# Performance work log

Measured on AMD Instinct MI355X. Metric: run time of the kernel, lower is better.

## Reference

```python
import jax, jax.numpy as jnp
import numpy as np

SQRT_HALF = np.float32(np.sqrt(0.5))


def _weight_norm(v, g):
    # torch weight_norm dim=0: per-output-row normalization, w = g * v / ||v||_row
    return (g / jnp.linalg.norm(v, axis=1))[:, None] * v


def setup_inputs() -> dict:
    key = jax.random.key(0)
    ks = jax.random.split(key, 6)
    B, L, C, E, H, W = 32, 1024, 1024, 1024, 14, 14
    return {
        "x": jax.random.normal(ks[0], (B, L, C), dtype=jnp.float32),
        "word_embed": jax.random.normal(ks[1], (B, L, E), dtype=jnp.float32),
        "conv_feats": jax.random.normal(ks[2], (B, E, H, W), dtype=jnp.float32),
        "in_v": jax.random.normal(ks[3], (E, C), dtype=jnp.float32) * np.float32(1.0 / np.sqrt(C)),
        "in_g": jnp.ones((E,), dtype=jnp.float32),
        "in_b": jnp.zeros((E,), dtype=jnp.float32),
        "out_v": jax.random.normal(ks[4], (C, E), dtype=jnp.float32) * np.float32(1.0 / np.sqrt(E)),
        "out_g": jnp.ones((C,), dtype=jnp.float32),
        "out_b": jnp.zeros((C,), dtype=jnp.float32),
    }


def reference(x, word_embed, conv_feats, in_v, in_g, in_b, out_v, out_g, out_b):
    # in_projection (weight-normed linear) + word_embed, scaled
    Wi = _weight_norm(in_v, in_g)                      # [E, C]
    h = (jnp.einsum('blc,ec->ble', x, Wi) + in_b + word_embed) * SQRT_HALF  # [B, L, E]

    B, E, H, W = conv_feats.shape
    n = H * W
    y = conv_feats.reshape(B, E, n)                    # [B, E, n]
    scores = jnp.einsum('ble,bev->blv', h, y)          # [B, L, n]
    attn = jax.nn.softmax(scores, axis=-1)             # [B, L, n]
    ctx = jnp.einsum('blv,bev->ble', attn, y)          # [B, L, E]
    ctx = ctx * jnp.asarray(n * np.sqrt(1.0 / n), dtype=ctx.dtype)  # = sqrt(n)

    # out_projection + residual, scaled
    Wo = _weight_norm(out_v, out_g)                    # [C, E]
    out = (jnp.einsum('ble,ce->blc', ctx, Wo) + out_b + x) * SQRT_HALF  # [B, L, C]
    return out, attn
```

## Files before the change

### kernel.cpp

```cpp
#include <hip/hip_runtime.h>
#include <hip/hip_bf16.h>

typedef unsigned short u16;
typedef _Float16 f16x8 __attribute__((ext_vector_type(8)));
typedef unsigned short u16x8 __attribute__((ext_vector_type(8)));
typedef float f32x4 __attribute__((ext_vector_type(4)));

#define SQHF 0.70710678118654752440f

__device__ __forceinline__ u16 f2h(float f) {
  const _Float16 h = (_Float16)f;
  return __builtin_bit_cast(u16, h);
}

template <int N>
__device__ __forceinline__ void vmwait() {
  asm volatile("s_waitcnt vmcnt(%0)" ::"i"(N) : "memory");
}

__device__ __forceinline__ void gload_lds16(const void* g, void* l) {
  __builtin_amdgcn_global_load_lds(
      (const __attribute__((address_space(1))) unsigned int*)g,
      (__attribute__((address_space(3))) unsigned int*)l, 16, 0, 0);
}

__device__ __forceinline__ float block_sum(float v) {
#pragma unroll
  for (int o = 32; o; o >>= 1) v += __shfl_xor(v, o);
  __shared__ float red[4];
  if ((threadIdx.x & 63) == 0) red[threadIdx.x >> 6] = v;
  __syncthreads();
  return red[0] + red[1] + red[2] + red[3];
}

__global__ void wnorm_t_kernel(const float* __restrict__ v, const float* __restrict__ g,
                               u16* __restrict__ wtf) {
  const int e = blockIdx.x;
  const float* vr = v + (long)e * 1024;
  float ss = 0.f;
  for (int c = threadIdx.x; c < 1024; c += 256) { float t = vr[c]; ss += t * t; }
  const float tot = block_sum(ss);
  const float scl = g[e] / sqrtf(tot);
  for (int c = threadIdx.x; c < 1024; c += 256) wtf[(long)c * 1024 + e] = f2h(vr[c] * scl);
}

__global__ void wnorm_kernel(const float* __restrict__ v, const float* __restrict__ g,
                             u16* __restrict__ w) {
  const int c = blockIdx.x;
  const float* vr = v + (long)c * 1024;
  float ss = 0.f;
  for (int e = threadIdx.x; e < 1024; e += 256) { float t = vr[e]; ss += t * t; }
  const float tot = block_sum(ss);
  const float scl = g[c] / sqrtf(tot);
  for (int e = threadIdx.x; e < 1024; e += 256) w[(long)c * 1024 + e] = f2h(vr[e] * scl);
}

__global__ void prep_y_kernel(const float* __restrict__ conv, const float* __restrict__ in_b,
                              u16* __restrict__ concat, float* __restrict__ rc) {
  const int b = blockIdx.x >> 4;
  const int e0 = (blockIdx.x & 15) << 6;
  __shared__ float tile[64 * 224];
  const float* cb = conv + ((long)b * 1024 + e0) * 196;
  for (int idx = threadIdx.x; idx < 64 * 224; idx += 256) {
    const int rr = idx / 224, vv = idx - rr * 224;
    tile[idx] = (vv < 196) ? cb[(long)rr * 196 + vv] : 0.f;
  }
  __syncthreads();
  for (int idx = threadIdx.x; idx < 256 * 64; idx += 256) {
    const int vr = idx >> 6, c = idx & 63;
    const float val = (vr < 224) ? tile[c * 224 + vr] : 0.f;
    concat[((long)b * 256 + vr) * 2048 + 1024 + e0 + c] = f2h(val);
  }
  const int v = threadIdx.x;
  if (v < 196) {
    float s = 0.f;
#pragma unroll 8
    for (int rr = 0; rr < 64; ++rr) s += in_b[e0 + rr] * tile[rr * 224 + v];
    atomicAdd(&rc[b * 256 + v], s);
  }
}

__global__ void softmax_kernel(const float* __restrict__ s0b, const float* __restrict__ s1b,
                               const float* __restrict__ rc,
                               float* __restrict__ attn, u16* __restrict__ attn_f) {
  const long row = (long)blockIdx.x * 4 + (threadIdx.x >> 6);
  const int lane = threadIdx.x & 63;
  const int b = (int)(row >> 10);
  const float* s0 = s0b + row * 256;
  const float* s1 = s1b + row * 256;
  const float* rcb = rc + b * 256;
  float v0 = (s0[lane] + s1[lane] + rcb[lane]) * SQHF;
  float v1 = (s0[64 + lane] + s1[64 + lane] + rcb[64 + lane]) * SQHF;
  float v2 = (s0[128 + lane] + s1[128 + lane] + rcb[128 + lane]) * SQHF;
  float v3 = (lane < 4) ? (s0[192 + lane] + s1[192 + lane] + rcb[192 + lane]) * SQHF : -1e30f;
  float mx = fmaxf(fmaxf(v0, v1), fmaxf(v2, v3));
#pragma unroll
  for (int o = 32; o; o >>= 1) mx = fmaxf(mx, __shfl_xor(mx, o));
  const float e0 = __expf(v0 - mx), e1 = __expf(v1 - mx), e2 = __expf(v2 - mx);
  const float e3 = (lane < 4) ? __expf(v3 - mx) : 0.f;
  float sm = e0 + e1 + e2 + e3;
#pragma unroll
  for (int o = 32; o; o >>= 1) sm += __shfl_xor(sm, o);
  const float inv = 1.f / sm;
  float* arow = attn + row * 196;
  arow[lane] = e0 * inv;
  arow[64 + lane] = e1 * inv;
  arow[128 + lane] = e2 * inv;
  if (lane < 4) arow[192 + lane] = e3 * inv;
  u16* brow = attn_f + row * 256;
  brow[lane] = f2h(e0 * inv);
  brow[64 + lane] = f2h(e1 * inv);
  brow[128 + lane] = f2h(e2 * inv);
  brow[192 + lane] = (lane < 4) ? f2h(e3 * inv) : (u16)0;
}

template <int EPI, int MODE>
__global__ __launch_bounds__(256) void gemm128(
    const u16* __restrict__ Ah,
    const float* __restrict__ Af0, const float* __restrict__ Af1, int kSw,
    const u16* __restrict__ Bh,
    int N, int K, int ldA, int ldB, int ldOut,
    int mTilesPerBatch, long bStride, int aTilesMod, int kSplit2,
    const float* __restrict__ bias, const float* __restrict__ extra,
    float scale, void* __restrict__ out1, void* __restrict__ out2) {
  constexpr int AREG = (MODE == 2);
  constexpr int TBH = 4096;
  constexpr int HSM = 8192;
  __shared__ __align__(16) u16 smem[HSM * 2];

  int bid = blockIdx.x, nwg = gridDim.x, half = 0;
  if (kSplit2) { half = bid & 1; bid >>= 1; nwg >>= 1; }
  const int kOff = half << 10;

  const int numN = N >> 7;
  const int q = nwg >> 3, r = nwg & 7, xcd = bid & 7, l8 = bid >> 3;
  const int wg = (xcd < r ? xcd * (q + 1) : r * (q + 1) + (xcd - r) * q) + l8;
  const int mTile = wg / numN, nTile = wg - mTile * numN;
  const long rowBase = (long)mTile << 7;
  const int colBase = nTile << 7;
  const int aTile = aTilesMod ? (mTile % aTilesMod) : mTile;
  const long aRowBase = (long)aTile << 7;
  const long bOff = mTilesPerBatch ? (long)(mTile / mTilesPerBatch) * bStride : 0;

  const u16* Agh = AREG ? nullptr : (Ah + aRowBase * ldA);
  const u16* Bgh = Bh + bOff + (long)colBase * ldB;

  const int tid = threadIdx.x;
  const int wave = tid >> 6, lane = tid & 63;
  const int wr = wave >> 1, wc = wave & 1;
  const int sr = wave * 16 + (lane >> 2);
  const int scS = (((lane & 3) ^ ((sr >> 1) & 3)) << 3);
  const int lr = lane & 15;

  f32x4 acc[4][4];
#pragma unroll
  for (int m = 0; m < 4; ++m)
#pragma unroll
    for (int n = 0; n < 4; ++n) acc[m][n] = f32x4{0.f, 0.f, 0.f, 0.f};

  auto stageB = [&](int buf, int k0) {
    u16* sb = smem + buf * HSM;
#pragma unroll
    for (int i = 0; i < 2; ++i) {
      const long ro = (long)(i * 64 + sr) * ldB + k0 + kOff + scS;
      gload_lds16(Bgh + ro, &sb[TBH + i * 2048 + wave * 512]);
    }
  };
  auto stageA_lds = [&](int buf, int k0) {
    u16* sb = smem + buf * HSM;
#pragma unroll
    for (int i = 0; i < 2; ++i) {
      const long ro = (long)(i * 64 + sr) * ldA + k0 + kOff + scS;
      gload_lds16(Agh + ro, &sb[i * 2048 + wave * 512]);
    }
  };

  auto compute = [&](int buf) {
    const u16* sb = smem + buf * HSM;
    f16x8 fa[4], fb[4];
#pragma unroll
    for (int m = 0; m < 4; ++m) {
      const int row = wr * 64 + m * 16 + lr;
      const int off = row * 32 + (((lane >> 4) ^ ((row >> 1) & 3)) << 3);
      fa[m] = __builtin_bit_cast(f16x8, *(const u16x8*)&sb[off]);
    }
#pragma unroll
    for (int n = 0; n < 4; ++n) {
      const int row = wc * 64 + n * 16 + lr;
      const int off = row * 32 + (((lane >> 4) ^ ((row >> 1) & 3)) << 3);
      fb[n] = __builtin_bit_cast(f16x8, *(const u16x8*)&sb[TBH + off]);
    }
    __builtin_amdgcn_s_setprio(1);
#pragma unroll
    for (int m = 0; m < 4; ++m)
#pragma unroll
      for (int n = 0; n < 4; ++n)
        acc[m][n] = __builtin_amdgcn_mfma_f32_16x16x32_f16(fa[m], fb[n], acc[m][n], 0, 0, 0);
    __builtin_amdgcn_s_setprio(0);
  };

  const int nSteps = K >> 5;

  if constexpr (AREG) {
    const int arow = tid >> 2, akch = tid & 3;
    const int r1 = arow + 64;
    const int aoff0 = arow * 32 + ((akch ^ ((arow >> 1) & 3)) << 3);
    const int aoff1 = r1 * 32 + ((akch ^ ((r1 >> 1) & 3)) << 3);
    f32x4 ra0, ra1, rb0, rb1;
    auto issueA = [&](int k0) {
      const int gk = k0 + kOff;
      const float* As = (gk < kSw) ? (Af0 + aRowBase * (long)ldA + gk)
                                   : (Af1 + aRowBase * (long)ldA + (gk - kSw));
      const float* p0 = As + (long)arow * ldA + akch * 8;
      const float* p1 = As + (long)r1 * ldA + akch * 8;
      ra0 = *(const f32x4*)p0; ra1 = *(const f32x4*)(p0 + 4);
      rb0 = *(const f32x4*)p1; rb1 = *(const f32x4*)(p1 + 4);
    };
    auto writeA = [&](int buf) {
      u16* sb = smem + buf * HSM;
      u16x8 w0, w1;
      w0[0] = f2h(ra0[0]); w0[1] = f2h(ra0[1]); w0[2] = f2h(ra0[2]); w0[3] = f2h(ra0[3]);
      w0[4] = f2h(ra1[0]); w0[5] = f2h(ra1[1]); w0[6] = f2h(ra1[2]); w0[7] = f2h(ra1[3]);
      w1[0] = f2h(rb0[0]); w1[1] = f2h(rb0[1]); w1[2] = f2h(rb0[2]); w1[3] = f2h(rb0[3]);
      w1[4] = f2h(rb1[0]); w1[5] = f2h(rb1[1]); w1[6] = f2h(rb1[2]); w1[7] = f2h(rb1[3]);
      *(u16x8*)&sb[aoff0] = w0;
      *(u16x8*)&sb[aoff1] = w1;
    };
    issueA(0); stageB(0, 0);
    vmwait<2>();
    writeA(0);
    if (nSteps > 1) { issueA(32); stageB(1, 32); }
    for (int t = 0; t < nSteps; ++t) {
      if (t + 1 < nSteps) {
        asm volatile("s_waitcnt vmcnt(6) lgkmcnt(0)" ::: "memory");
      } else {
        asm volatile("s_waitcnt vmcnt(0) lgkmcnt(0)" ::: "memory");
      }
      __builtin_amdgcn_s_barrier();
      __builtin_amdgcn_sched_barrier(0);
      compute(t & 1);
      __builtin_amdgcn_sched_barrier(0);
      __builtin_amdgcn_s_barrier();
      if (t + 1 < nSteps) {
        vmwait<2>();
        writeA((t + 1) & 1);
        if (t + 2 < nSteps) { issueA((t + 2) << 5); stageB(t & 1, (t + 2) << 5); }
      }
    }
  } else {
    stageA_lds(0, 0); stageB(0, 0);
    for (int t = 0; t < nSteps; ++t) {
      const int cur = t & 1;
      if (t + 1 < nSteps) {
        stageA_lds(cur ^ 1, (t + 1) << 5);
        stageB(cur ^ 1, (t + 1) << 5);
        vmwait<4>();
      } else {
        vmwait<0>();
      }
      __builtin_amdgcn_s_barrier();
      __builtin_amdgcn_sched_barrier(0);
      compute(cur);
      __builtin_amdgcn_sched_barrier(0);
      __builtin_amdgcn_s_barrier();
    }
  }

  const int rloc = (lane >> 4) << 2;
  float* o3 = (float*)(half ? out2 : out1);
#pragma unroll
  for (int m = 0; m < 4; ++m) {
#pragma unroll
    for (int n = 0; n < 4; ++n) {
      const int col = colBase + wc * 64 + n * 16 + lr;
#pragma unroll
      for (int j = 0; j < 4; ++j) {
        const long row = rowBase + wr * 64 + m * 16 + rloc + j;
        const float v = acc[m][n][j];
        if (EPI == 1) {
          ((float*)out1)[row * (long)ldOut + col] =
              (v + bias[col] + extra[row * (long)ldOut + col]) * scale;
        } else if (EPI == 3) {
          o3[row * (long)ldOut + col] = v;
        } else if (EPI == 6) {
          ((u16*)out1)[row * (long)ldOut + col] = f2h(v * scale);
        }
      }
    }
  }
}

extern "C" void kernel_launch(void* const* d_in, const int* in_sizes, int n_in,
                              void* d_out, int out_size, void* d_ws, size_t ws_size,
                              hipStream_t stream) {
  (void)in_sizes; (void)n_in; (void)out_size; (void)ws_size;
  const float* x     = (const float*)d_in[0];
  const float* we    = (const float*)d_in[1];
  const float* conv  = (const float*)d_in[2];
  const float* in_v  = (const float*)d_in[3];
  const float* in_g  = (const float*)d_in[4];
  const float* in_b  = (const float*)d_in[5];
  const float* out_v = (const float*)d_in[6];
  const float* out_g = (const float*)d_in[7];
  const float* out_b = (const float*)d_in[8];
  float* out  = (float*)d_out;
  float* attn = out + 33554432l;

  char* ws = (char*)d_ws;
  u16* concat = (u16*)(ws);
  u16* wtf    = (u16*)(ws + 33554432l);
  u16* wo     = (u16*)(ws + 35651584l);
  u16* zo     = (u16*)(ws + 37748736l);
  u16* attf   = (u16*)(ws + 54525952l);
  float* rc   = (float*)(ws + 71303168l);
  float* s1   = (float*)(ws + 71368704l);
  float* s0   = out;

  hipMemsetAsync(rc, 0, 32 * 256 * sizeof(float), stream);
  wnorm_t_kernel<<<1024, 256, 0, stream>>>(in_v, in_g, wtf);
  wnorm_kernel<<<1024, 256, 0, stream>>>(out_v, out_g, wo);
  prep_y_kernel<<<512, 256, 0, stream>>>(conv, in_b, concat, rc);
  gemm128<6, 3><<<512, 256, 0, stream>>>(
      concat + 1024, nullptr, nullptr, 0, wtf,
      1024, 1024, 2048, 1024, 2048, 0, 0, 0, 0, nullptr, nullptr, 1.f, concat, nullptr);
  gemm128<3, 2><<<1024, 256, 0, stream>>>(
      nullptr, x, we, 1024, concat,
      256, 1024, 1024, 2048, 256, 8, 524288l, 0, 1, nullptr, nullptr, 1.f, s0, s1);
  softmax_kernel<<<8192, 256, 0, stream>>>(s0, s1, rc, attn, attf);
  gemm128<6, 3><<<512, 256, 0, stream>>>(
      wo, nullptr, nullptr, 0, concat + 1024,
      256, 1024, 1024, 2048, 256, 8, 524288l, 8, 0, nullptr, nullptr, 14.f, zo, nullptr);
  gemm128<1, 3><<<2048, 256, 0, stream>>>(
      attf, nullptr, nullptr, 0, zo,
      1024, 256, 256, 256, 1024, 8, 262144l, 0, 0, out_b, x, SQHF, out, nullptr);
}
```

Measured before the change: 307.5 us.

## Add dedicated 256x256-tile scores GEMM so fp32 x/word_embed are read once

Replaces the generic 128x128 split-K scores GEMM with a specialised 512-thread kernel using 256-row by 256-column tiles. Each workgroup now covers all 256 score columns, so the fp32 activations x and word_embed are loaded and converted to fp16 only once instead of twice. The generic gemm128 template drops its register-A path and split-K mode, which is a cleanup. In exchange the new kernel uses 64KB of LDS and 128 accumulator floats per thread, which lowers occupancy and gives only 256 workgroups.

Result: faster. 290.8 us (-5.5%).

```diff
diff --git a/kernel.cpp b/kernel.cpp
--- a/kernel.cpp
+++ b/kernel.cpp
@@ -114,24 +114,155 @@
   brow[192 + lane] = (lane < 4) ? f2h(e3 * inv) : (u16)0;
 }
 
-template <int EPI, int MODE>
+__global__ __launch_bounds__(512) void gemm_scores(
+    const float* __restrict__ Af0, const float* __restrict__ Af1,
+    const u16* __restrict__ Bh, long bStride,
+    float* __restrict__ out0, float* __restrict__ out1) {
+  constexpr int TBH = 8192;
+  constexpr int HSM = 16384;
+  __shared__ __align__(16) u16 smem[HSM * 2];
+
+  int bid = blockIdx.x;
+  const int half = bid & 1;
+  bid >>= 1;
+  const int nwg = gridDim.x >> 1;
+  const int q = nwg >> 3, xcd = bid & 7, l8 = bid >> 3;
+  const int mTile = xcd * q + l8;
+  const long rowBase = (long)mTile << 8;
+  const int kOff = half << 10;
+
+  const long bOff = (long)(mTile >> 2) * bStride;
+  const u16* Bg = Bh + bOff;
+
+  const int tid = threadIdx.x;
+  const int wave = tid >> 6, lane = tid & 63;
+  const int wr = wave >> 2, wc = wave & 3;
+  const int lr = lane & 15;
+
+  const int sbr = tid >> 2;
+  const int sbc = tid & 3;
+  const int arow = tid >> 1, akch = tid & 1;
+  const int aswz = (arow >> 1) & 3;
+  const int aoff0 = arow * 32 + ((akch ^ aswz) << 3);
+  const int aoff1 = arow * 32 + (((akch + 2) ^ aswz) << 3);
+
+  f32x4 acc[8][4];
+#pragma unroll
+  for (int m = 0; m < 8; ++m)
+#pragma unroll
+    for (int n = 0; n < 4; ++n) acc[m][n] = f32x4{0.f, 0.f, 0.f, 0.f};
+
+  f32x4 ra0, ra1, rb0, rb1;
+  auto issueA = [&](int k0) {
+    const int gk = k0 + kOff;
+    const float* As = (gk < 1024) ? (Af0 + rowBase * 1024 + gk)
+                                  : (Af1 + rowBase * 1024 + (gk - 1024));
+    const float* p = As + (long)arow * 1024 + akch * 8;
+    ra0 = *(const f32x4*)p;        ra1 = *(const f32x4*)(p + 4);
+    rb0 = *(const f32x4*)(p + 16); rb1 = *(const f32x4*)(p + 20);
+  };
+  auto writeA = [&](int buf) {
+    u16* sb = smem + buf * HSM;
+    u16x8 w0, w1;
+    w0[0] = f2h(ra0[0]); w0[1] = f2h(ra0[1]); w0[2] = f2h(ra0[2]); w0[3] = f2h(ra0[3]);
+    w0[4] = f2h(ra1[0]); w0[5] = f2h(ra1[1]); w0[6] = f2h(ra1[2]); w0[7] = f2h(ra1[3]);
+    w1[0] = f2h(rb0[0]); w1[1] = f2h(rb0[1]); w1[2] = f2h(rb0[2]); w1[3] = f2h(rb0[3]);
+    w1[4] = f2h(rb1[0]); w1[5] = f2h(rb1[1]); w1[6] = f2h(rb1[2]); w1[7] = f2h(rb1[3]);
+    *(u16x8*)&sb[aoff0] = w0;
+    *(u16x8*)&sb[aoff1] = w1;
+  };
+  auto stageB = [&](int buf, int k0) {
+    u16* sb = smem + buf * HSM;
+#pragma unroll
+    for (int i = 0; i < 2; ++i) {
+      const int row = i * 128 + sbr;
+      const int csw = ((sbc ^ ((row >> 1) & 3)) << 3);
+      gload_lds16(Bg + (long)row * 2048 + k0 + kOff + csw,
+                  &smem[buf * HSM + TBH + i * 4096 + wave * 512]);
+      (void)sb;
+    }
+  };
+
+  auto compute = [&](int buf) {
+    const u16* sb = smem + buf * HSM;
+    f16x8 fb[4];
+#pragma unroll
+    for (int n = 0; n < 4; ++n) {
+      const int row = wc * 64 + n * 16 + lr;
+      const int off = TBH + row * 32 + (((lane >> 4) ^ ((row >> 1) & 3)) << 3);
+      fb[n] = __builtin_bit_cast(f16x8, *(const u16x8*)&sb[off]);
+    }
+#pragma unroll
+    for (int h = 0; h < 2; ++h) {
+      f16x8 fa[4];
+#pragma unroll
+      for (int m = 0; m < 4; ++m) {
+        const int row = wr * 128 + (h * 4 + m) * 16 + lr;
+        const int off = row * 32 + (((lane >> 4) ^ ((row >> 1) & 3)) << 3);
+        fa[m] = __builtin_bit_cast(f16x8, *(const u16x8*)&sb[off]);
+      }
+      __builtin_amdgcn_s_setprio(1);
+#pragma unroll
+      for (int m = 0; m < 4; ++m)
+#pragma unroll
+        for (int n = 0; n < 4; ++n)
+          acc[h * 4 + m][n] =
+              __builtin_amdgcn_mfma_f32_16x16x32_f16(fa[m], fb[n], acc[h * 4 + m][n], 0, 0, 0);
+      __builtin_amdgcn_s_setprio(0);
+    }
+  };
+
+  const int nSteps = 32;
+  issueA(0); stageB(0, 0);
+  vmwait<2>();
+  writeA(0);
+  issueA(32); stageB(1, 32);
+  for (int t = 0; t < nSteps; ++t) {
+    if (t + 1 < nSteps) {
+      asm volatile("s_waitcnt vmcnt(6) lgkmcnt(0)" ::: "memory");
+    } else {
+      asm volatile("s_waitcnt vmcnt(0) lgkmcnt(0)" ::: "memory");
+    }
+    __builtin_amdgcn_s_barrier();
+    __builtin_amdgcn_sched_barrier(0);
+    compute(t & 1);
+    __builtin_amdgcn_sched_barrier(0);
+    __builtin_amdgcn_s_barrier();
+    if (t + 1 < nSteps) {
+      vmwait<2>();
+      writeA((t + 1) & 1);
+      if (t + 2 < nSteps) { issueA((t + 2) << 5); stageB(t & 1, (t + 2) << 5); }
+    }
+  }
+
+  float* o = half ? out1 : out0;
+  const int rloc = (lane >> 4) << 2;
+#pragma unroll
+  for (int m = 0; m < 8; ++m) {
+#pragma unroll
+    for (int n = 0; n < 4; ++n) {
+      const int col = wc * 64 + n * 16 + lr;
+#pragma unroll
+      for (int j = 0; j < 4; ++j) {
+        const long row = rowBase + wr * 128 + m * 16 + rloc + j;
+        o[row * 256 + col] = acc[m][n][j];
+      }
+    }
+  }
+}
+
+template <int EPI>
 __global__ __launch_bounds__(256) void gemm128(
-    const u16* __restrict__ Ah,
-    const float* __restrict__ Af0, const float* __restrict__ Af1, int kSw,
-    const u16* __restrict__ Bh,
+    const u16* __restrict__ Ah, const u16* __restrict__ Bh,
     int N, int K, int ldA, int ldB, int ldOut,
-    int mTilesPerBatch, long bStride, int aTilesMod, int kSplit2,
+    int mTilesPerBatch, long bStride, int aTilesMod,
     const float* __restrict__ bias, const float* __restrict__ extra,
-    float scale, void* __restrict__ out1, void* __restrict__ out2) {
-  constexpr int AREG = (MODE == 2);
+    float scale, void* __restrict__ out1) {
   constexpr int TBH = 4096;
   constexpr int HSM = 8192;
   __shared__ __align__(16) u16 smem[HSM * 2];
 
-  int bid = blockIdx.x, nwg = gridDim.x, half = 0;
-  if (kSplit2) { half = bid & 1; bid >>= 1; nwg >>= 1; }
-  const int kOff = half << 10;
-
+  const int bid = blockIdx.x, nwg = gridDim.x;
   const int numN = N >> 7;
   const int q = nwg >> 3, r = nwg & 7, xcd = bid & 7, l8 = bid >> 3;
   const int wg = (xcd < r ? xcd * (q + 1) : r * (q + 1) + (xcd - r) * q) + l8;
@@ -142,7 +273,7 @@
   const long aRowBase = (long)aTile << 7;
   const long bOff = mTilesPerBatch ? (long)(mTile / mTilesPerBatch) * bStride : 0;
 
-  const u16* Agh = AREG ? nullptr : (Ah + aRowBase * ldA);
+  const u16* Agh = Ah + aRowBase * ldA;
   const u16* Bgh = Bh + bOff + (long)colBase * ldB;
 
   const int tid = threadIdx.x;
@@ -158,20 +289,15 @@
 #pragma unroll
     for (int n = 0; n < 4; ++n) acc[m][n] = f32x4{0.f, 0.f, 0.f, 0.f};
 
-  auto stageB = [&](int buf, int k0) {
+  auto stage = [&](int buf, int k0) {
     u16* sb = smem + buf * HSM;
 #pragma unroll
     for (int i = 0; i < 2; ++i) {
-      const long ro = (long)(i * 64 + sr) * ldB + k0 + kOff + scS;
-      gload_lds16(Bgh + ro, &sb[TBH + i * 2048 + wave * 512]);
-    }
-  };
-  auto stageA_lds = [&](int buf, int k0) {
-    u16* sb = smem + buf * HSM;
-#pragma unroll
-    for (int i = 0; i < 2; ++i) {
-      const long ro = (long)(i * 64 + sr) * ldA + k0 + kOff + scS;
-      gload_lds16(Agh + ro, &sb[i * 2048 + wave * 512]);
+      const long roA = (long)(i * 64 + sr) * ldA + k0 + scS;
+      const long roB = (long)(i * 64 + sr) * ldB + k0 + scS;
+      const int lo_ = i * 2048 + wave * 512;
+      gload_lds16(Agh + roA, &sb[lo_]);
+      gload_lds16(Bgh + roB, &sb[TBH + lo_]);
     }
   };
 
@@ -200,74 +326,23 @@
   };
 
   const int nSteps = K >> 5;
-
-  if constexpr (AREG) {
-    const int arow = tid >> 2, akch = tid & 3;
-    const int r1 = arow + 64;
-    const int aoff0 = arow * 32 + ((akch ^ ((arow >> 1) & 3)) << 3);
-    const int aoff1 = r1 * 32 + ((akch ^ ((r1 >> 1) & 3)) << 3);
-    f32x4 ra0, ra1, rb0, rb1;
-    auto issueA = [&](int k0) {
-      const int gk = k0 + kOff;
-      const float* As = (gk < kSw) ? (Af0 + aRowBase * (long)ldA + gk)
-                                   : (Af1 + aRowBase * (long)ldA + (gk - kSw));
-      const float* p0 = As + (long)arow * ldA + akch * 8;
-      const float* p1 = As + (long)r1 * ldA + akch * 8;
-      ra0 = *(const f32x4*)p0; ra1 = *(const f32x4*)(p0 + 4);
-      rb0 = *(const f32x4*)p1; rb1 = *(const f32x4*)(p1 + 4);
-    };
-    auto writeA = [&](int buf) {
-      u16* sb = smem + buf * HSM;
-      u16x8 w0, w1;
-      w0[0] = f2h(ra0[0]); w0[1] = f2h(ra0[1]); w0[2] = f2h(ra0[2]); w0[3] = f2h(ra0[3]);
-      w0[4] = f2h(ra1[0]); w0[5] = f2h(ra1[1]); w0[6] = f2h(ra1[2]); w0[7] = f2h(ra1[3]);
-      w1[0] = f2h(rb0[0]); w1[1] = f2h(rb0[1]); w1[2] = f2h(rb0[2]); w1[3] = f2h(rb0[3]);
-      w1[4] = f2h(rb1[0]); w1[5] = f2h(rb1[1]); w1[6] = f2h(rb1[2]); w1[7] = f2h(rb1[3]);
-      *(u16x8*)&sb[aoff0] = w0;
-      *(u16x8*)&sb[aoff1] = w1;
-    };
-    issueA(0); stageB(0, 0);
-    vmwait<2>();
-    writeA(0);
-    if (nSteps > 1) { issueA(32); stageB(1, 32); }
-    for (int t = 0; t < nSteps; ++t) {
-      if (t + 1 < nSteps) {
-        asm volatile("s_waitcnt vmcnt(6) lgkmcnt(0)" ::: "memory");
-      } else {
-        asm volatile("s_waitcnt vmcnt(0) lgkmcnt(0)" ::: "memory");
-      }
-      __builtin_amdgcn_s_barrier();
-      __builtin_amdgcn_sched_barrier(0);
-      compute(t & 1);
-      __builtin_amdgcn_sched_barrier(0);
-      __builtin_amdgcn_s_barrier();
-      if (t + 1 < nSteps) {
-        vmwait<2>();
-        writeA((t + 1) & 1);
-        if (t + 2 < nSteps) { issueA((t + 2) << 5); stageB(t & 1, (t + 2) << 5); }
-      }
-    }
-  } else {
-    stageA_lds(0, 0); stageB(0, 0);
-    for (int t = 0; t < nSteps; ++t) {
-      const int cur = t & 1;
-      if (t + 1 < nSteps) {
-        stageA_lds(cur ^ 1, (t + 1) << 5);
-        stageB(cur ^ 1, (t + 1) << 5);
-        vmwait<4>();
-      } else {
-        vmwait<0>();
-      }
-      __builtin_amdgcn_s_barrier();
-      __builtin_amdgcn_sched_barrier(0);
-      compute(cur);
-      __builtin_amdgcn_sched_barrier(0);
-      __builtin_amdgcn_s_barrier();
-    }
+  stage(0, 0);
+  for (int t = 0; t < nSteps; ++t) {
+    const int cur = t & 1;
+    if (t + 1 < nSteps) {
+      stage(cur ^ 1, (t + 1) << 5);
+      vmwait<4>();
+    } else {
+      vmwait<0>();
+    }
+    __builtin_amdgcn_s_barrier();
+    __builtin_amdgcn_sched_barrier(0);
+    compute(cur);
+    __builtin_amdgcn_sched_barrier(0);
+    __builtin_amdgcn_s_barrier();
   }
 
   const int rloc = (lane >> 4) << 2;
-  float* o3 = (float*)(half ? out2 : out1);
 #pragma unroll
   for (int m = 0; m < 4; ++m) {
 #pragma unroll
@@ -280,8 +355,6 @@
         if (EPI == 1) {
           ((float*)out1)[row * (long)ldOut + col] =
               (v + bias[col] + extra[row * (long)ldOut + col]) * scale;
-        } else if (EPI == 3) {
-          o3[row * (long)ldOut + col] = v;
         } else if (EPI == 6) {
           ((u16*)out1)[row * (long)ldOut + col] = f2h(v * scale);
         }
@@ -320,17 +393,15 @@
   wnorm_t_kernel<<<1024, 256, 0, stream>>>(in_v, in_g, wtf);
   wnorm_kernel<<<1024, 256, 0, stream>>>(out_v, out_g, wo);
   prep_y_kernel<<<512, 256, 0, stream>>>(conv, in_b, concat, rc);
-  gemm128<6, 3><<<512, 256, 0, stream>>>(
-      concat + 1024, nullptr, nullptr, 0, wtf,
-      1024, 1024, 2048, 1024, 2048, 0, 0, 0, 0, nullptr, nullptr, 1.f, concat, nullptr);
-  gemm128<3, 2><<<1024, 256, 0, stream>>>(
-      nullptr, x, we, 1024, concat,
-      256, 1024, 1024, 2048, 256, 8, 524288l, 0, 1, nullptr, nullptr, 1.f, s0, s1);
+  gemm128<6><<<512, 256, 0, stream>>>(
+      concat + 1024, wtf, 1024, 1024, 2048, 1024, 2048,
+      0, 0, 0, nullptr, nullptr, 1.f, concat);
+  gemm_scores<<<256, 512, 0, stream>>>(x, we, concat, 524288l, s0, s1);
   softmax_kernel<<<8192, 256, 0, stream>>>(s0, s1, rc, attn, attf);
-  gemm128<6, 3><<<512, 256, 0, stream>>>(
-      wo, nullptr, nullptr, 0, concat + 1024,
-      256, 1024, 1024, 2048, 256, 8, 524288l, 8, 0, nullptr, nullptr, 14.f, zo, nullptr);
-  gemm128<1, 3><<<2048, 256, 0, stream>>>(
-      attf, nullptr, nullptr, 0, zo,
-      1024, 256, 256, 256, 1024, 8, 262144l, 0, 0, out_b, x, SQHF, out, nullptr);
-}
+  gemm128<6><<<512, 256, 0, stream>>>(
+      wo, concat + 1024, 256, 1024, 1024, 2048, 256,
+      8, 524288l, 8, nullptr, nullptr, 14.f, zo);
+  gemm128<1><<<2048, 256, 0, stream>>>(
+      attf, zo, 1024, 256, 256, 256, 1024,
+      8, 262144l, 0, out_b, x, SQHF, out);
+}
```
